# Optimization experiments

Hardware: AMD Instinct MI355X
Metric: run time of the kernel (lower is better)

## Reference

```python
import jax, jax.numpy as jnp
import numpy as np

N = 100000      # num nodes
E = 1600000     # num edges
F_IN = 128      # feature_dim
H = 128         # hidden_channels
B = 8192        # num link queries


def setup_inputs() -> dict:
    key = jax.random.key(0)
    ks = jax.random.split(key, 13)
    x = jax.random.normal(ks[0], (N, F_IN), dtype=jnp.float32)
    edge_index = jax.random.randint(ks[1], (2, E), 0, N, dtype=jnp.int32)
    root_n_index = jax.random.randint(ks[2], (B, 2), 0, N, dtype=jnp.int32)
    s = 1.0 / np.sqrt(H).astype(np.float32)
    W1 = jax.random.normal(ks[3], (F_IN, H), jnp.float32) * s
    b1 = jnp.zeros((H,), jnp.float32)
    W2 = jax.random.normal(ks[4], (H, H), jnp.float32) * s
    b2 = jnp.zeros((H,), jnp.float32)
    W3 = jax.random.normal(ks[5], (H, H), jnp.float32) * s
    b3 = jnp.zeros((H,), jnp.float32)
    P1 = jax.random.normal(ks[6], (H, H), jnp.float32) * s
    pb1 = jnp.zeros((H,), jnp.float32)
    P2 = jax.random.normal(ks[7], (H, 1), jnp.float32) * s
    pb2 = jnp.zeros((1,), jnp.float32)
    return {"x": x, "edge_index": edge_index, "root_n_index": root_n_index,
            "W1": W1, "b1": b1, "W2": W2, "b2": b2, "W3": W3, "b3": b3,
            "P1": P1, "pb1": pb1, "P2": P2, "pb2": pb2}


def gcn_conv(h, src, dst, norm, W, b):
    # transform then gather-scale-scatter: out = D^-1/2 (A+I) D^-1/2 (h W) + b
    h = h @ W                                  # [N, H]
    msg = h[src] * norm[:, None]               # [E+N, H]
    return jax.ops.segment_sum(msg, dst, num_segments=N) + b


def reference(x, edge_index, root_n_index, W1, b1, W2, b2, W3, b3, P1, pb1, P2, pb2):
    # add self loops (GCNConv default) and compute symmetric normalization once
    loop = jnp.arange(N, dtype=edge_index.dtype)
    src = jnp.concatenate([edge_index[0], loop])
    dst = jnp.concatenate([edge_index[1], loop])
    deg = jax.ops.segment_sum(jnp.ones_like(dst, jnp.float32), dst, num_segments=N)
    dinv = jnp.where(deg > 0, jax.lax.rsqrt(jnp.maximum(deg, 1.0)), 0.0)
    norm = dinv[src] * dinv[dst]

    # 3 stacked GCN layers; dropout is identity in eval mode
    h = jax.nn.relu(gcn_conv(x, src, dst, norm, W1, b1))
    h = jax.nn.relu(gcn_conv(h, src, dst, norm, W2, b2))
    h = gcn_conv(h, src, dst, norm, W3, b3)

    # link embeddings: elementwise product of src/dst node embeddings
    link = h[root_n_index[:, 0]] * h[root_n_index[:, 1]]   # [B, H]
    link = jax.nn.relu(link @ P1 + pb1)
    logits = (link @ P2 + pb2).squeeze(-1)                 # [B]
    return logits
```

## Files before the change

kernel.cpp:

```cpp
#include <hip/hip_runtime.h>

#define NN 100000
#define EE 1600000
#define HH 128
#define BB 8192
#define SCAN_NBLK ((NN + 1023) / 1024)


__global__ void hist_kernel(const int* __restrict__ dst, int* __restrict__ hist) {
    int e = blockIdx.x * blockDim.x + threadIdx.x;
    if (e < EE) atomicAdd(&hist[dst[e]], 1);
}

__global__ void dinv_kernel(const int* __restrict__ hist, float* __restrict__ dinv) {
    int i = blockIdx.x * blockDim.x + threadIdx.x;
    if (i < NN) dinv[i] = rsqrtf((float)hist[i] + 1.0f);
}

__global__ __launch_bounds__(1024) void scan_partial_kernel(const int* __restrict__ hist,
        int* __restrict__ bsum) {
    __shared__ int red[1024];
    int i = blockIdx.x * 1024 + threadIdx.x;
    int v = (i < NN) ? hist[i] : 0;
    red[threadIdx.x] = v;
    __syncthreads();
    for (int d = 512; d > 0; d >>= 1) {
        if (threadIdx.x < d) red[threadIdx.x] += red[threadIdx.x + d];
        __syncthreads();
    }
    if (threadIdx.x == 0) bsum[blockIdx.x] = red[0];
}

__global__ void scan_sums_kernel(const int* __restrict__ bsum, int* __restrict__ bbase) {
    int acc = 0;
    for (int b = 0; b < SCAN_NBLK; ++b) { bbase[b] = acc; acc += bsum[b]; }
    bbase[SCAN_NBLK] = acc;
}

__global__ __launch_bounds__(1024) void scan_offs_kernel(const int* __restrict__ hist,
        const int* __restrict__ bbase, int* __restrict__ offs, int* __restrict__ cursor) {
    __shared__ int sc[1024];
    int i = blockIdx.x * 1024 + threadIdx.x;
    int v = (i < NN) ? hist[i] : 0;
    sc[threadIdx.x] = v;
    __syncthreads();
    for (int d = 1; d < 1024; d <<= 1) {
        int t = (threadIdx.x >= d) ? sc[threadIdx.x - d] : 0;
        __syncthreads();
        sc[threadIdx.x] += t;
        __syncthreads();
    }
    if (i < NN) {
        int excl = bbase[blockIdx.x] + sc[threadIdx.x] - v;
        offs[i] = excl;
        cursor[i] = excl;
        if (i == NN - 1) offs[NN] = excl + v;
    }
}

__global__ void fill_kernel(const int* __restrict__ src, const int* __restrict__ dst,
        const float* __restrict__ dinv, int* __restrict__ cursor,
        int* __restrict__ esrc, float* __restrict__ enorm) {
    int e = blockIdx.x * blockDim.x + threadIdx.x;
    if (e >= EE) return;
    int s = src[e], d = dst[e];
    int p = atomicAdd(&cursor[d], 1);
    esrc[p] = s;
    enorm[p] = dinv[s] * dinv[d];
}


__global__ __launch_bounds__(256) void gemm128(const float* __restrict__ A,
        const float* __restrict__ W, const float* __restrict__ bias,
        float* __restrict__ C, int M, int relu) {
    __shared__ float4 As4[16 * 128];
    __shared__ float4 Ws4[64 * 32];
    const int tid = threadIdx.x;
    const int row0 = blockIdx.x * 128;
    const int tcol8 = tid & 15;
    const int trowg = tid >> 4;

    float acc[8][8];
#pragma unroll
    for (int r = 0; r < 8; ++r)
#pragma unroll
        for (int c = 0; c < 8; ++c) acc[r][c] = 0.f;

    const float4* A4 = (const float4*)A;
    const float4* W4 = (const float4*)W;

    for (int kc = 0; kc < 128; kc += 64) {
        __syncthreads();
#pragma unroll
        for (int i = 0; i < 8; ++i) {
            int p = tid + 256 * i;
            int row = p >> 4, k4 = p & 15;
            int gr = row0 + row;
            float4 v = make_float4(0.f, 0.f, 0.f, 0.f);
            if (gr < M) v = A4[(size_t)gr * 32 + (kc >> 2) + k4];
            As4[k4 * 128 + row] = v;
        }
#pragma unroll
        for (int i = 0; i < 8; ++i) {
            int p = tid + 256 * i;
            Ws4[p] = W4[(size_t)kc * 32 + p];
        }
        __syncthreads();

#pragma unroll
        for (int k4 = 0; k4 < 16; ++k4) {
            float4 a[8];
#pragma unroll
            for (int r = 0; r < 8; ++r)
                a[r] = As4[k4 * 128 + trowg + 16 * r];
#pragma unroll
            for (int kk = 0; kk < 4; ++kk) {
                int k = k4 * 4 + kk;
                float4 w0 = Ws4[k * 32 + tcol8 * 2];
                float4 w1 = Ws4[k * 32 + tcol8 * 2 + 1];
#pragma unroll
                for (int r = 0; r < 8; ++r) {
                    float av = (kk == 0) ? a[r].x : (kk == 1) ? a[r].y
                             : (kk == 2) ? a[r].z : a[r].w;
                    acc[r][0] += av * w0.x; acc[r][1] += av * w0.y;
                    acc[r][2] += av * w0.z; acc[r][3] += av * w0.w;
                    acc[r][4] += av * w1.x; acc[r][5] += av * w1.y;
                    acc[r][6] += av * w1.z; acc[r][7] += av * w1.w;
                }
            }
        }
    }

    float bv[8];
#pragma unroll
    for (int c = 0; c < 8; ++c) bv[c] = 0.f;
    if (bias) {
        float4 b0 = ((const float4*)bias)[tcol8 * 2];
        float4 b1 = ((const float4*)bias)[tcol8 * 2 + 1];
        bv[0] = b0.x; bv[1] = b0.y; bv[2] = b0.z; bv[3] = b0.w;
        bv[4] = b1.x; bv[5] = b1.y; bv[6] = b1.z; bv[7] = b1.w;
    }
    float4* C4 = (float4*)C;
#pragma unroll
    for (int r = 0; r < 8; ++r) {
        int gr = row0 + trowg + 16 * r;
        if (gr < M) {
            float o[8];
#pragma unroll
            for (int c = 0; c < 8; ++c) {
                float v = acc[r][c] + bv[c];
                o[c] = relu ? fmaxf(v, 0.f) : v;
            }
            C4[(size_t)gr * 32 + tcol8 * 2]     = make_float4(o[0], o[1], o[2], o[3]);
            C4[(size_t)gr * 32 + tcol8 * 2 + 1] = make_float4(o[4], o[5], o[6], o[7]);
        }
    }
}


__global__ __launch_bounds__(256) void agg_kernel(const float* __restrict__ t,
        float* __restrict__ out, const int* __restrict__ offs,
        const int* __restrict__ esrc, const float* __restrict__ enorm,
        const float* __restrict__ dinv, const float* __restrict__ bias, int relu) {
    const int wave = threadIdx.x >> 6;
    const int lane = threadIdx.x & 63;
    const int node = blockIdx.x * 4 + wave;
    if (node >= NN) return;
    const int half = lane >> 5;
    const int hl = lane & 31;

    const float4* t4 = (const float4*)t;
    float ax = 0.f, ay = 0.f, az = 0.f, aw = 0.f;

    if (half == 0) {
        float di = dinv[node];
        float s = di * di;
        float4 sv = t4[(size_t)node * 32 + hl];
        ax = sv.x * s; ay = sv.y * s; az = sv.z * s; aw = sv.w * s;
    }

    int e = offs[node];
    const int e1 = offs[node + 1];
    for (; e + 8 <= e1; e += 8) {
        int i0 = e + half,     i1 = e + 2 + half;
        int i2 = e + 4 + half, i3 = e + 6 + half;
        int s0 = esrc[i0], s1 = esrc[i1], s2 = esrc[i2], s3 = esrc[i3];
        float n0 = enorm[i0], n1 = enorm[i1], n2 = enorm[i2], n3 = enorm[i3];
        float4 v0 = t4[(size_t)s0 * 32 + hl];
        float4 v1 = t4[(size_t)s1 * 32 + hl];
        float4 v2 = t4[(size_t)s2 * 32 + hl];
        float4 v3 = t4[(size_t)s3 * 32 + hl];
        ax += v0.x * n0; ay += v0.y * n0; az += v0.z * n0; aw += v0.w * n0;
        ax += v1.x * n1; ay += v1.y * n1; az += v1.z * n1; aw += v1.w * n1;
        ax += v2.x * n2; ay += v2.y * n2; az += v2.z * n2; aw += v2.w * n2;
        ax += v3.x * n3; ay += v3.y * n3; az += v3.z * n3; aw += v3.w * n3;
    }
    for (; e + 2 <= e1; e += 2) {
        int ee = e + half;
        int s = esrc[ee];
        float nm = enorm[ee];
        float4 v = t4[(size_t)s * 32 + hl];
        ax += v.x * nm; ay += v.y * nm; az += v.z * nm; aw += v.w * nm;
    }
    if (e < e1 && half == 0) {
        int s = esrc[e];
        float nm = enorm[e];
        float4 v = t4[(size_t)s * 32 + hl];
        ax += v.x * nm; ay += v.y * nm; az += v.z * nm; aw += v.w * nm;
    }

    ax += __shfl_xor(ax, 32); ay += __shfl_xor(ay, 32);
    az += __shfl_xor(az, 32); aw += __shfl_xor(aw, 32);

    if (half == 0) {
        if (bias) {
            float4 b = ((const float4*)bias)[hl];
            ax += b.x; ay += b.y; az += b.z; aw += b.w;
        }
        if (relu) {
            ax = fmaxf(ax, 0.f); ay = fmaxf(ay, 0.f);
            az = fmaxf(az, 0.f); aw = fmaxf(aw, 0.f);
        }
        ((float4*)out)[(size_t)node * 32 + hl] = make_float4(ax, ay, az, aw);
    }
}


__global__ __launch_bounds__(256) void link_kernel(const float* __restrict__ h,
        const int* __restrict__ roots, float* __restrict__ linkb) {
    const int wave = threadIdx.x >> 6;
    const int lane = threadIdx.x & 63;
    const int b = blockIdx.x * 4 + wave;
    if (b >= BB) return;
    const int f = lane * 2;
    int r0 = roots[b * 2], r1 = roots[b * 2 + 1];
    float2 u = *(const float2*)&h[(size_t)r0 * HH + f];
    float2 v = *(const float2*)&h[(size_t)r1 * HH + f];
    *(float2*)&linkb[(size_t)b * HH + f] = make_float2(u.x * v.x, u.y * v.y);
}

__global__ __launch_bounds__(256) void logits_kernel(const float* __restrict__ g,
        const float* __restrict__ P2, const float* __restrict__ pb2,
        float* __restrict__ out) {
    const int wave = threadIdx.x >> 6;
    const int lane = threadIdx.x & 63;
    const int b = blockIdx.x * 4 + wave;
    if (b >= BB) return;
    const int f = lane * 2;
    float2 gv = *(const float2*)&g[(size_t)b * HH + f];
    float2 pv = *(const float2*)&P2[f];
    float s = gv.x * pv.x + gv.y * pv.y;
    for (int off = 32; off > 0; off >>= 1) s += __shfl_down(s, off);
    if (lane == 0) out[b] = s + pb2[0];
}


extern "C" void kernel_launch(void* const* d_in, const int* in_sizes, int n_in,
                              void* d_out, int out_size, void* d_ws, size_t ws_size,
                              hipStream_t stream) {
    const float* x   = (const float*)d_in[0];
    const int*   ei  = (const int*)d_in[1];
    const int* roots = (const int*)d_in[2];
    const float* W1  = (const float*)d_in[3];
    const float* b1  = (const float*)d_in[4];
    const float* W2  = (const float*)d_in[5];
    const float* b2  = (const float*)d_in[6];
    const float* W3  = (const float*)d_in[7];
    const float* b3  = (const float*)d_in[8];
    const float* P1  = (const float*)d_in[9];
    const float* pb1 = (const float*)d_in[10];
    const float* P2  = (const float*)d_in[11];
    const float* pb2 = (const float*)d_in[12];
    float* out = (float*)d_out;
    (void)in_sizes; (void)n_in; (void)out_size; (void)ws_size;

    char* ws = (char*)d_ws;
    size_t woff = 0;
    auto alloc = [&](size_t bytes) {
        void* p = ws + woff;
        woff += (bytes + 255) & ~(size_t)255;
        return p;
    };
    int*   hist   = (int*)  alloc((size_t)NN * 4);
    float* dinv   = (float*)alloc((size_t)NN * 4);
    int*   offs   = (int*)  alloc((size_t)(NN + 1) * 4);
    int*   cursor = (int*)  alloc((size_t)NN * 4);
    int*   bsum   = (int*)  alloc((size_t)(SCAN_NBLK + 1) * 4);
    int*   bbase  = (int*)  alloc((size_t)(SCAN_NBLK + 1) * 4);
    int*   esrc   = (int*)  alloc((size_t)EE * 4);
    float* enorm  = (float*)alloc((size_t)EE * 4);
    float* bufA   = (float*)alloc((size_t)NN * HH * 4);
    float* bufB   = (float*)alloc((size_t)NN * HH * 4);
    float* linkb  = (float*)alloc((size_t)BB * HH * 4);
    float* gout   = (float*)alloc((size_t)BB * HH * 4);

    const int* e_src = ei;
    const int* e_dst = ei + EE;

    hipMemsetAsync(hist, 0, (size_t)NN * 4, stream);
    hist_kernel<<<(EE + 255) / 256, 256, 0, stream>>>(e_dst, hist);
    dinv_kernel<<<(NN + 255) / 256, 256, 0, stream>>>(hist, dinv);
    scan_partial_kernel<<<SCAN_NBLK, 1024, 0, stream>>>(hist, bsum);
    scan_sums_kernel<<<1, 1, 0, stream>>>(bsum, bbase);
    scan_offs_kernel<<<SCAN_NBLK, 1024, 0, stream>>>(hist, bbase, offs, cursor);
    fill_kernel<<<(EE + 255) / 256, 256, 0, stream>>>(e_src, e_dst, dinv, cursor, esrc, enorm);

    gemm128<<<(NN + 127) / 128, 256, 0, stream>>>(x, W1, nullptr, bufA, NN, 0);
    agg_kernel<<<(NN + 3) / 4, 256, 0, stream>>>(bufA, bufB, offs, esrc, enorm, dinv, b1, 1);
    gemm128<<<(NN + 127) / 128, 256, 0, stream>>>(bufB, W2, nullptr, bufA, NN, 0);
    agg_kernel<<<(NN + 3) / 4, 256, 0, stream>>>(bufA, bufB, offs, esrc, enorm, dinv, b2, 1);
    gemm128<<<(NN + 127) / 128, 256, 0, stream>>>(bufB, W3, nullptr, bufA, NN, 0);
    agg_kernel<<<(NN + 3) / 4, 256, 0, stream>>>(bufA, bufB, offs, esrc, enorm, dinv, b3, 0);

    link_kernel<<<(BB + 3) / 4, 256, 0, stream>>>(bufB, roots, linkb);
    gemm128<<<(BB + 127) / 128, 256, 0, stream>>>(linkb, P1, pb1, gout, BB, 1);
    logits_kernel<<<(BB + 3) / 4, 256, 0, stream>>>(gout, P2, pb2, out);
}
```

Measured before the change: 896.2 us.

## Replace FP32 SIMT GEMM with split-bf16 MFMA GEMM using pre-split weights

The scalar FP32 128x128 GEMM is replaced with a matrix-core kernel. Activations are split on the fly into bf16 hi/lo pairs in LDS, and weights are pre-split and packed into an MFMA fragment layout by a small kernel. Three bf16 MFMAs per tile (hh, hl, lh) approximate FP32 accuracy. This targets the ALU-bound dense transforms, at the cost of extra split work, four small extra launches, and scattered scalar output stores.

```diff
diff --git a/kernel.cpp b/kernel.cpp
--- a/kernel.cpp
+++ b/kernel.cpp
@@ -5,6 +5,18 @@
 #define HH 128
 #define BB 8192
 #define SCAN_NBLK ((NN + 1023) / 1024)
+#define LDA 136
+
+typedef __attribute__((ext_vector_type(8))) short bf16x8;
+typedef __attribute__((ext_vector_type(4))) float f32x4;
+
+__device__ __forceinline__ void split2(float a, ushort& hi, ushort& lo) {
+    unsigned u = __float_as_uint(a);
+    hi = (ushort)(u >> 16);
+    float hf = __uint_as_float(u & 0xFFFF0000u);
+    float l = a - hf;
+    lo = (ushort)(__float_as_uint(l) >> 16);
+}
 
 
 __global__ void hist_kernel(const int* __restrict__ dst, int* __restrict__ hist) {
@@ -70,89 +82,113 @@
 }
 
 
-__global__ __launch_bounds__(256) void gemm128(const float* __restrict__ A,
-        const float* __restrict__ W, const float* __restrict__ bias,
+__global__ __launch_bounds__(256) void wsplit_kernel(const float* __restrict__ W,
+        short* __restrict__ Wf) {
+    int e = blockIdx.x * 256 + threadIdx.x;
+    int kind = e >> 11;
+    int k0 = (e >> 9) & 3;
+    int ct = (e >> 6) & 7;
+    int l = e & 63;
+    int kb = k0 * 32 + (l >> 4) * 8;
+    int c = ct * 16 + (l & 15);
+    short v[8];
+#pragma unroll
+    for (int j = 0; j < 8; ++j) {
+        float w = W[(size_t)(kb + j) * HH + c];
+        ushort hi, lo;
+        split2(w, hi, lo);
+        v[j] = (short)(kind ? lo : hi);
+    }
+    bf16x8 pack;
+#pragma unroll
+    for (int j = 0; j < 8; ++j) pack[j] = v[j];
+    *(bf16x8*)(Wf + (size_t)e * 8) = pack;
+}
+
+
+__global__ __launch_bounds__(256) void gemm_mfma(const float* __restrict__ A,
+        const short* __restrict__ Wf, const float* __restrict__ bias,
         float* __restrict__ C, int M, int relu) {
-    __shared__ float4 As4[16 * 128];
-    __shared__ float4 Ws4[64 * 32];
+    __shared__ short Ah[128 * LDA];
+    __shared__ short Al[128 * LDA];
     const int tid = threadIdx.x;
     const int row0 = blockIdx.x * 128;
-    const int tcol8 = tid & 15;
-    const int trowg = tid >> 4;
-
-    float acc[8][8];
-#pragma unroll
-    for (int r = 0; r < 8; ++r)
-#pragma unroll
-        for (int c = 0; c < 8; ++c) acc[r][c] = 0.f;
 
     const float4* A4 = (const float4*)A;
-    const float4* W4 = (const float4*)W;
-
-    for (int kc = 0; kc < 128; kc += 64) {
-        __syncthreads();
-#pragma unroll
-        for (int i = 0; i < 8; ++i) {
-            int p = tid + 256 * i;
-            int row = p >> 4, k4 = p & 15;
-            int gr = row0 + row;
-            float4 v = make_float4(0.f, 0.f, 0.f, 0.f);
-            if (gr < M) v = A4[(size_t)gr * 32 + (kc >> 2) + k4];
-            As4[k4 * 128 + row] = v;
-        }
-#pragma unroll
-        for (int i = 0; i < 8; ++i) {
-            int p = tid + 256 * i;
-            Ws4[p] = W4[(size_t)kc * 32 + p];
-        }
-        __syncthreads();
-
-#pragma unroll
-        for (int k4 = 0; k4 < 16; ++k4) {
-            float4 a[8];
-#pragma unroll
-            for (int r = 0; r < 8; ++r)
-                a[r] = As4[k4 * 128 + trowg + 16 * r];
-#pragma unroll
-            for (int kk = 0; kk < 4; ++kk) {
-                int k = k4 * 4 + kk;
-                float4 w0 = Ws4[k * 32 + tcol8 * 2];
-                float4 w1 = Ws4[k * 32 + tcol8 * 2 + 1];
-#pragma unroll
-                for (int r = 0; r < 8; ++r) {
-                    float av = (kk == 0) ? a[r].x : (kk == 1) ? a[r].y
-                             : (kk == 2) ? a[r].z : a[r].w;
-                    acc[r][0] += av * w0.x; acc[r][1] += av * w0.y;
-                    acc[r][2] += av * w0.z; acc[r][3] += av * w0.w;
-                    acc[r][4] += av * w1.x; acc[r][5] += av * w1.y;
-                    acc[r][6] += av * w1.z; acc[r][7] += av * w1.w;
+#pragma unroll
+    for (int i = 0; i < 16; ++i) {
+        int p = i * 256 + tid;
+        int row = p >> 5, k4 = p & 31;
+        int gr = row0 + row;
+        float4 v = make_float4(0.f, 0.f, 0.f, 0.f);
+        if (gr < M) v = A4[(size_t)gr * 32 + k4];
+        ushort h0, l0, h1, l1, h2, l2, h3, l3;
+        split2(v.x, h0, l0); split2(v.y, h1, l1);
+        split2(v.z, h2, l2); split2(v.w, h3, l3);
+        *(short4*)&Ah[row * LDA + k4 * 4] =
+            make_short4((short)h0, (short)h1, (short)h2, (short)h3);
+        *(short4*)&Al[row * LDA + k4 * 4] =
+            make_short4((short)l0, (short)l1, (short)l2, (short)l3);
+    }
+    __syncthreads();
+
+    const int lane = tid & 63;
+    const int wave = tid >> 6;
+    const int wr0 = wave * 32;
+    const int arow = lane & 15;
+    const int koff = (lane >> 4) * 8;
+
+    f32x4 acc[2][8];
+#pragma unroll
+    for (int rt = 0; rt < 2; ++rt)
+#pragma unroll
+        for (int ct = 0; ct < 8; ++ct)
+#pragma unroll
+            for (int m = 0; m < 4; ++m) acc[rt][ct][m] = 0.f;
+
+    for (int k0 = 0; k0 < 4; ++k0) {
+        bf16x8 wh[8], wl[8];
+#pragma unroll
+        for (int ct = 0; ct < 8; ++ct) {
+            wh[ct] = *(const bf16x8*)(Wf + ((size_t)(k0 * 8 + ct) * 64 + lane) * 8);
+            wl[ct] = *(const bf16x8*)(Wf + ((size_t)(2048 + k0 * 512 + ct * 64 + lane)) * 8);
+        }
+        bf16x8 ah[2], al[2];
+#pragma unroll
+        for (int rt = 0; rt < 2; ++rt) {
+            int r = wr0 + rt * 16 + arow;
+            ah[rt] = *(const bf16x8*)&Ah[r * LDA + k0 * 32 + koff];
+            al[rt] = *(const bf16x8*)&Al[r * LDA + k0 * 32 + koff];
+        }
+#pragma unroll
+        for (int rt = 0; rt < 2; ++rt)
+#pragma unroll
+            for (int ct = 0; ct < 8; ++ct) {
+                acc[rt][ct] = __builtin_amdgcn_mfma_f32_16x16x32_bf16(
+                    ah[rt], wh[ct], acc[rt][ct], 0, 0, 0);
+                acc[rt][ct] = __builtin_amdgcn_mfma_f32_16x16x32_bf16(
+                    ah[rt], wl[ct], acc[rt][ct], 0, 0, 0);
+                acc[rt][ct] = __builtin_amdgcn_mfma_f32_16x16x32_bf16(
+                    al[rt], wh[ct], acc[rt][ct], 0, 0, 0);
+            }
+    }
+
+    const int ccol = lane & 15;
+    const int crow = (lane >> 4) * 4;
+#pragma unroll
+    for (int ct = 0; ct < 8; ++ct) {
+        float bv = bias ? bias[ct * 16 + ccol] : 0.f;
+#pragma unroll
+        for (int rt = 0; rt < 2; ++rt) {
+#pragma unroll
+            for (int m = 0; m < 4; ++m) {
+                int gr = row0 + wr0 + rt * 16 + crow + m;
+                if (gr < M) {
+                    float v = acc[rt][ct][m] + bv;
+                    if (relu) v = fmaxf(v, 0.f);
+                    C[(size_t)gr * HH + ct * 16 + ccol] = v;
                 }
             }
-        }
-    }
-
-    float bv[8];
-#pragma unroll
-    for (int c = 0; c < 8; ++c) bv[c] = 0.f;
-    if (bias) {
-        float4 b0 = ((const float4*)bias)[tcol8 * 2];
-        float4 b1 = ((const float4*)bias)[tcol8 * 2 + 1];
-        bv[0] = b0.x; bv[1] = b0.y; bv[2] = b0.z; bv[3] = b0.w;
-        bv[4] = b1.x; bv[5] = b1.y; bv[6] = b1.z; bv[7] = b1.w;
-    }
-    float4* C4 = (float4*)C;
-#pragma unroll
-    for (int r = 0; r < 8; ++r) {
-        int gr = row0 + trowg + 16 * r;
-        if (gr < M) {
-            float o[8];
-#pragma unroll
-            for (int c = 0; c < 8; ++c) {
-                float v = acc[r][c] + bv[c];
-                o[c] = relu ? fmaxf(v, 0.f) : v;
-            }
-            C4[(size_t)gr * 32 + tcol8 * 2]     = make_float4(o[0], o[1], o[2], o[3]);
-            C4[(size_t)gr * 32 + tcol8 * 2 + 1] = make_float4(o[4], o[5], o[6], o[7]);
         }
     }
 }
@@ -182,8 +218,7 @@
     int e = offs[node];
     const int e1 = offs[node + 1];
     for (; e + 8 <= e1; e += 8) {
-        int i0 = e + half,     i1 = e + 2 + half;
-        int i2 = e + 4 + half, i3 = e + 6 + half;
+        int i0 = e + half, i1 = e + 2 + half, i2 = e + 4 + half, i3 = e + 6 + half;
         int s0 = esrc[i0], s1 = esrc[i1], s2 = esrc[i2], s3 = esrc[i3];
         float n0 = enorm[i0], n1 = enorm[i1], n2 = enorm[i2], n3 = enorm[i3];
         float4 v0 = t4[(size_t)s0 * 32 + hl];
@@ -293,6 +328,10 @@
     float* bufB   = (float*)alloc((size_t)NN * HH * 4);
     float* linkb  = (float*)alloc((size_t)BB * HH * 4);
     float* gout   = (float*)alloc((size_t)BB * HH * 4);
+    short* Wf1    = (short*)alloc((size_t)4096 * 8 * 2);
+    short* Wf2    = (short*)alloc((size_t)4096 * 8 * 2);
+    short* Wf3    = (short*)alloc((size_t)4096 * 8 * 2);
+    short* WfP1   = (short*)alloc((size_t)4096 * 8 * 2);
 
     const int* e_src = ei;
     const int* e_dst = ei + EE;
@@ -305,14 +344,19 @@
     scan_offs_kernel<<<SCAN_NBLK, 1024, 0, stream>>>(hist, bbase, offs, cursor);
     fill_kernel<<<(EE + 255) / 256, 256, 0, stream>>>(e_src, e_dst, dinv, cursor, esrc, enorm);
 
-    gemm128<<<(NN + 127) / 128, 256, 0, stream>>>(x, W1, nullptr, bufA, NN, 0);
+    wsplit_kernel<<<16, 256, 0, stream>>>(W1, Wf1);
+    wsplit_kernel<<<16, 256, 0, stream>>>(W2, Wf2);
+    wsplit_kernel<<<16, 256, 0, stream>>>(W3, Wf3);
+    wsplit_kernel<<<16, 256, 0, stream>>>(P1, WfP1);
+
+    gemm_mfma<<<(NN + 127) / 128, 256, 0, stream>>>(x, Wf1, nullptr, bufA, NN, 0);
     agg_kernel<<<(NN + 3) / 4, 256, 0, stream>>>(bufA, bufB, offs, esrc, enorm, dinv, b1, 1);
-    gemm128<<<(NN + 127) / 128, 256, 0, stream>>>(bufB, W2, nullptr, bufA, NN, 0);
+    gemm_mfma<<<(NN + 127) / 128, 256, 0, stream>>>(bufB, Wf2, nullptr, bufA, NN, 0);
     agg_kernel<<<(NN + 3) / 4, 256, 0, stream>>>(bufA, bufB, offs, esrc, enorm, dinv, b2, 1);
-    gemm128<<<(NN + 127) / 128, 256, 0, stream>>>(bufB, W3, nullptr, bufA, NN, 0);
+    gemm_mfma<<<(NN + 127) / 128, 256, 0, stream>>>(bufB, Wf3, nullptr, bufA, NN, 0);
     agg_kernel<<<(NN + 3) / 4, 256, 0, stream>>>(bufA, bufB, offs, esrc, enorm, dinv, b3, 0);
 
     link_kernel<<<(BB + 3) / 4, 256, 0, stream>>>(bufB, roots, linkb);
-    gemm128<<<(BB + 127) / 128, 256, 0, stream>>>(linkb, P1, pb1, gout, BB, 1);
+    gemm_mfma<<<(BB + 127) / 128, 256, 0, stream>>>(linkb, WfP1, pb1, gout, BB, 1);
     logits_kernel<<<(BB + 3) / 4, 256, 0, stream>>>(gout, P2, pb2, out);
 }
```

Measured after the change: 780.7 us. -12.9%, faster.
